# Optimization experiments

Measured on AMD Instinct MI355X. Metric: run time of the kernel, lower is better.

The kernel has to match this reference:

```python
import jax, jax.numpy as jnp
import numpy as np

EPS = 1e-07

def ternary_quantize(w, gamma=1.0):
    # gamma' = gamma / (mean|W| + eps)
    w_bar = jnp.mean(jnp.abs(w))
    gamma_prime = gamma / (w_bar + EPS)
    q = jnp.where(w > 0.5, 1.0, jnp.where(w < -0.5, -1.0, 0.0)).astype(w.dtype)
    # RoundClip(gamma' * q, -1, 1); jnp.round matches torch.round (half-to-even)
    return jnp.clip(jnp.round(gamma_prime * q), -1.0, 1.0)

def setup_inputs() -> dict:
    key = jax.random.key(0)
    kx, kw = jax.random.split(key)
    x = jax.random.normal(kx, (4, 2048, 4096), dtype=jnp.float32)
    weight = jax.random.normal(kw, (4096, 4096), dtype=jnp.float32)  # [out, in]
    return {"x": x, "weight": weight}

def reference(x, weight):
    wq = ternary_quantize(weight)
    # F.linear: x @ W^T
    return jnp.einsum('bsi,oi->bso', x, wq)
```

## Files before the change

### kernel.cpp

```cpp
#include <hip/hip_runtime.h>
#include <hip/hip_bf16.h>
#include <stdint.h>


typedef __bf16 bf16x8 __attribute__((ext_vector_type(8)));
typedef float  f32x4  __attribute__((ext_vector_type(4)));

#define EPS 1e-7f
#define NPART 4096

__device__ __forceinline__ void async_load16(const void* g, void* l) {
    __builtin_amdgcn_global_load_lds(
        (__attribute__((address_space(1))) void*)(const_cast<void*>(g)),
        (__attribute__((address_space(3))) void*)l,
        16, 0, 0);
}

__device__ __forceinline__ unsigned short f2bf_rne(float f) {
    unsigned u = __float_as_uint(f);
    unsigned r = (u + 0x7fffu + ((u >> 16) & 1u)) >> 16;
    return (unsigned short)r;
}

__device__ __forceinline__ float scale_from_partials(const float* __restrict__ partials,
                                                     float invCount) {
    const int lane = threadIdx.x & 63;
    const float4* p4 = (const float4*)partials;
    float s = 0.0f;
    #pragma unroll
    for (int j = 0; j < NPART / 4 / 64; ++j) {
        float4 v = p4[lane + 64 * j];
        s += v.x + v.y + v.z + v.w;
    }
    #pragma unroll
    for (int off = 32; off > 0; off >>= 1) s += __shfl_down(s, off, 64);
    s = __shfl(s, 0, 64);
    float mean = s * invCount;
    float gp = 1.0f / (mean + EPS);
    return fminf(fmaxf(rintf(gp), -1.0f), 1.0f);
}


__device__ __forceinline__ unsigned short tern_bf16(float w) {
    return (w > 0.5f) ? (unsigned short)0x3F80u
         : ((w < -0.5f) ? (unsigned short)0xBF80u : (unsigned short)0u);
}

__global__ __launch_bounds__(256) void quant_w_bf16(
    const float* __restrict__ in, ushort4* __restrict__ out,
    float* __restrict__ partials, int n4)
{
    int tid = blockIdx.x * blockDim.x + threadIdx.x;
    int stride = gridDim.x * blockDim.x;
    float s = 0.0f;
    for (int i = tid; i < n4; i += stride) {
        float4 v = ((const float4*)in)[i];
        s += fabsf(v.x) + fabsf(v.y) + fabsf(v.z) + fabsf(v.w);
        ushort4 r;
        r.x = tern_bf16(v.x); r.y = tern_bf16(v.y);
        r.z = tern_bf16(v.z); r.w = tern_bf16(v.w);
        out[i] = r;
    }
    #pragma unroll
    for (int off = 32; off > 0; off >>= 1) s += __shfl_down(s, off, 64);
    __shared__ float psum[4];
    int lane = threadIdx.x & 63, wid = threadIdx.x >> 6;
    if (lane == 0) psum[wid] = s;
    __syncthreads();
    if (threadIdx.x == 0)
        partials[blockIdx.x] = psum[0] + psum[1] + psum[2] + psum[3];
}


__global__ __launch_bounds__(256) void conv_x_bf16(
    const float* __restrict__ in, ushort4* __restrict__ out, int n4)
{
    int i = blockIdx.x * blockDim.x + threadIdx.x;
    if (i < n4) {
        float4 v = ((const float4*)in)[i];
        ushort4 r;
        r.x = f2bf_rne(v.x); r.y = f2bf_rne(v.y);
        r.z = f2bf_rne(v.z); r.w = f2bf_rne(v.w);
        out[i] = r;
    }
}


#define BM 128
#define BN 128
#define BK 64

__global__ __launch_bounds__(256) void gemm_bt(
    const __bf16* __restrict__ A,
    const __bf16* __restrict__ B,
    float* __restrict__ C,
    const float* __restrict__ partials,
    int N, int K, float invCount)
{
    __shared__ __bf16 As[BM * BK];
    __shared__ __bf16 Bs[BN * BK];

    const int t    = threadIdx.x;
    const int lane = t & 63;
    const int wid  = t >> 6;
    const int mBase = blockIdx.y * BM;
    const int nBase = blockIdx.x * BN;
    const int wm = (wid >> 1) * 64;
    const int wn = (wid & 1) * 64;
    const int lm = lane & 15;
    const int quad = lane >> 4;
    const int lm7 = lm & 7;

    f32x4 acc[4][4] = {};

    const __bf16* gA = A + (size_t)mBase * K;
    const __bf16* gB = B + (size_t)nBase * K;

    for (int k0 = 0; k0 < K; k0 += BK) {
        #pragma unroll
        for (int i = 0; i < 4; ++i) {
            int ch = i * 256 + t;
            int row = ch >> 3, sc = ch & 7;
            int cc = sc ^ (row & 7);
            async_load16(gA + (size_t)row * K + k0 + cc * 8, &As[ch * 8]);
        }
        #pragma unroll
        for (int i = 0; i < 4; ++i) {
            int ch = i * 256 + t;
            int row = ch >> 3, sc = ch & 7;
            int cc = sc ^ (row & 7);
            async_load16(gB + (size_t)row * K + k0 + cc * 8, &Bs[ch * 8]);
        }
        __syncthreads();

        #pragma unroll
        for (int ks = 0; ks < BK; ks += 32) {
            const int cc = (ks >> 3) + quad;
            const int swz = cc ^ lm7;
            bf16x8 af[4], bfr[4];
            #pragma unroll
            for (int mt = 0; mt < 4; ++mt)
                af[mt] = *(const bf16x8*)&As[((wm + mt * 16 + lm) * 8 + swz) * 8];
            #pragma unroll
            for (int nt = 0; nt < 4; ++nt)
                bfr[nt] = *(const bf16x8*)&Bs[((wn + nt * 16 + lm) * 8 + swz) * 8];
            #pragma unroll
            for (int mt = 0; mt < 4; ++mt)
                #pragma unroll
                for (int nt = 0; nt < 4; ++nt)
                    acc[mt][nt] = __builtin_amdgcn_mfma_f32_16x16x32_bf16(
                        af[mt], bfr[nt], acc[mt][nt], 0, 0, 0);
        }
        __syncthreads();
    }

    const float tscale = scale_from_partials(partials, invCount);

    #pragma unroll
    for (int mt = 0; mt < 4; ++mt) {
        #pragma unroll
        for (int nt = 0; nt < 4; ++nt) {
            #pragma unroll
            for (int r = 0; r < 4; ++r) {
                int row = mBase + wm + mt * 16 + quad * 4 + r;
                int col = nBase + wn + nt * 16 + lm;
                C[(size_t)row * N + col] = tscale * acc[mt][nt][r];
            }
        }
    }
}


__global__ void gemm_fallback(const float* __restrict__ x, const float* __restrict__ w,
                              float* __restrict__ out, const float* __restrict__ partials,
                              int N, int K, float invCount)
{
    __shared__ float xs[16][17];
    __shared__ float qs[16][17];
    int tx = threadIdx.x & 15;
    int ty = threadIdx.x >> 4;
    int row = blockIdx.y * 16 + ty;
    int col = blockIdx.x * 16 + tx;
    float acc = 0.0f;
    for (int k0 = 0; k0 < K; k0 += 16) {
        xs[ty][tx] = x[(size_t)row * K + k0 + tx];
        float wv = w[(size_t)(blockIdx.x * 16 + ty) * K + k0 + tx];
        qs[ty][tx] = (wv > 0.5f) ? 1.0f : ((wv < -0.5f) ? -1.0f : 0.0f);
        __syncthreads();
        #pragma unroll
        for (int j = 0; j < 16; ++j) acc += xs[ty][j] * qs[tx][j];
        __syncthreads();
    }
    float tscale = scale_from_partials(partials, invCount);
    out[(size_t)row * N + col] = tscale * acc;
}

__global__ __launch_bounds__(256) void absmean_only(
    const float* __restrict__ w, float* __restrict__ partials, int n4)
{
    int tid = blockIdx.x * blockDim.x + threadIdx.x;
    int stride = gridDim.x * blockDim.x;
    float s = 0.0f;
    for (int i = tid; i < n4; i += stride) {
        float4 v = ((const float4*)w)[i];
        s += fabsf(v.x) + fabsf(v.y) + fabsf(v.z) + fabsf(v.w);
    }
    #pragma unroll
    for (int off = 32; off > 0; off >>= 1) s += __shfl_down(s, off, 64);
    __shared__ float psum[4];
    int lane = threadIdx.x & 63, wid = threadIdx.x >> 6;
    if (lane == 0) psum[wid] = s;
    __syncthreads();
    if (threadIdx.x == 0)
        partials[blockIdx.x] = psum[0] + psum[1] + psum[2] + psum[3];
}


extern "C" void kernel_launch(void* const* d_in, const int* in_sizes, int n_in,
                              void* d_out, int out_size, void* d_ws, size_t ws_size,
                              hipStream_t stream) {
    const float* x = (const float*)d_in[0];
    const float* w = (const float*)d_in[1];
    float* out = (float*)d_out;

    const int K = 4096;
    const int M = in_sizes[0] / K;
    const int N = in_sizes[1] / K;
    const float invCount = 1.0f / (float)(in_sizes[1]);

    float* partials = (float*)d_ws;
    const size_t base = NPART * sizeof(float);
    const size_t need = base + (size_t)M * K * 2 + (size_t)N * K * 2;

    if (ws_size >= need) {
        __bf16* xb = (__bf16*)((char*)d_ws + base);
        __bf16* qb = (__bf16*)((char*)d_ws + base + (size_t)M * K * 2);

        int xn4 = (M * K) / 4;
        int wn4 = (N * K) / 4;
        quant_w_bf16<<<NPART, 256, 0, stream>>>(w, (ushort4*)qb, partials, wn4);
        conv_x_bf16<<<(xn4 + 255) / 256, 256, 0, stream>>>(x, (ushort4*)xb, xn4);

        dim3 grid(N / BN, M / BM);
        gemm_bt<<<grid, 256, 0, stream>>>(xb, qb, out, partials, N, K, invCount);
    } else {
        absmean_only<<<NPART, 256, 0, stream>>>(w, partials, in_sizes[1] / 4);
        dim3 grid(N / 16, M / 16);
        gemm_fallback<<<grid, 256, 0, stream>>>(x, w, out, partials, N, K, invCount);
    }
}
```

Before: 570.2 us.

## Use 32x32 MFMA, XCD-aware tile remap, and fuse prep kernels

The GEMM inner loop now uses the 32x32x16 bf16 MFMA with a 2x2 tile per wave instead of 4x4 16x16x32 tiles. This cuts LDS fragment loads per MFMA and raises work per instruction. Workgroups are remapped so that each XCD handles a contiguous band of N panels, which should improve L2 reuse of the weight tiles. The weight quantization and x conversion kernels are merged into one grid-stride prep kernel, saving a launch at the cost of a fixed grid size for the x conversion.

After: 667.1 us. 17.0% more time.

```diff
diff --git a/kernel.cpp b/kernel.cpp
--- a/kernel.cpp
+++ b/kernel.cpp
@@ -3,8 +3,8 @@
 #include <stdint.h>
 
 
-typedef __bf16 bf16x8 __attribute__((ext_vector_type(8)));
-typedef float  f32x4  __attribute__((ext_vector_type(4)));
+typedef __bf16 bf16x8  __attribute__((ext_vector_type(8)));
+typedef float  f32x16  __attribute__((ext_vector_type(16)));
 
 #define EPS 1e-7f
 #define NPART 4096
@@ -40,26 +40,34 @@
     return fminf(fmaxf(rintf(gp), -1.0f), 1.0f);
 }
 
-
 __device__ __forceinline__ unsigned short tern_bf16(float w) {
     return (w > 0.5f) ? (unsigned short)0x3F80u
          : ((w < -0.5f) ? (unsigned short)0xBF80u : (unsigned short)0u);
 }
 
-__global__ __launch_bounds__(256) void quant_w_bf16(
-    const float* __restrict__ in, ushort4* __restrict__ out,
-    float* __restrict__ partials, int n4)
+
+__global__ __launch_bounds__(256) void prep(
+    const float* __restrict__ x, const float* __restrict__ w,
+    ushort4* __restrict__ xb, ushort4* __restrict__ qb,
+    float* __restrict__ partials, int xn4, int wn4)
 {
     int tid = blockIdx.x * blockDim.x + threadIdx.x;
     int stride = gridDim.x * blockDim.x;
     float s = 0.0f;
-    for (int i = tid; i < n4; i += stride) {
-        float4 v = ((const float4*)in)[i];
+    for (int i = tid; i < wn4; i += stride) {
+        float4 v = ((const float4*)w)[i];
         s += fabsf(v.x) + fabsf(v.y) + fabsf(v.z) + fabsf(v.w);
         ushort4 r;
         r.x = tern_bf16(v.x); r.y = tern_bf16(v.y);
         r.z = tern_bf16(v.z); r.w = tern_bf16(v.w);
-        out[i] = r;
+        qb[i] = r;
+    }
+    for (int i = tid; i < xn4; i += stride) {
+        float4 v = ((const float4*)x)[i];
+        ushort4 r;
+        r.x = f2bf_rne(v.x); r.y = f2bf_rne(v.y);
+        r.z = f2bf_rne(v.z); r.w = f2bf_rne(v.w);
+        xb[i] = r;
     }
     #pragma unroll
     for (int off = 32; off > 0; off >>= 1) s += __shfl_down(s, off, 64);
@@ -72,20 +80,6 @@
 }
 
 
-__global__ __launch_bounds__(256) void conv_x_bf16(
-    const float* __restrict__ in, ushort4* __restrict__ out, int n4)
-{
-    int i = blockIdx.x * blockDim.x + threadIdx.x;
-    if (i < n4) {
-        float4 v = ((const float4*)in)[i];
-        ushort4 r;
-        r.x = f2bf_rne(v.x); r.y = f2bf_rne(v.y);
-        r.z = f2bf_rne(v.z); r.w = f2bf_rne(v.w);
-        out[i] = r;
-    }
-}
-
-
 #define BM 128
 #define BN 128
 #define BK 64
@@ -95,7 +89,7 @@
     const __bf16* __restrict__ B,
     float* __restrict__ C,
     const float* __restrict__ partials,
-    int N, int K, float invCount)
+    int N, int K, float invCount, int mPan, int nPan)
 {
     __shared__ __bf16 As[BM * BK];
     __shared__ __bf16 Bs[BN * BK];
@@ -103,15 +97,27 @@
     const int t    = threadIdx.x;
     const int lane = t & 63;
     const int wid  = t >> 6;
-    const int mBase = blockIdx.y * BM;
-    const int nBase = blockIdx.x * BN;
+
+    int gid = blockIdx.y * gridDim.x + blockIdx.x;
+    int mIdx, nIdx;
+    if ((nPan & 7) == 0 && ((mPan * nPan) & 7) == 0) {
+        int xcd = gid & 7;
+        int local = gid >> 3;
+        mIdx = local % mPan;
+        nIdx = xcd * (nPan >> 3) + (local / mPan);
+    } else {
+        nIdx = gid % nPan;
+        mIdx = gid / nPan;
+    }
+
+    const int mBase = mIdx * BM;
+    const int nBase = nIdx * BN;
     const int wm = (wid >> 1) * 64;
     const int wn = (wid & 1) * 64;
-    const int lm = lane & 15;
-    const int quad = lane >> 4;
-    const int lm7 = lm & 7;
-
-    f32x4 acc[4][4] = {};
+    const int l31   = lane & 31;
+    const int khalf = lane >> 5;
+
+    f32x16 acc[2][2] = {};
 
     const __bf16* gA = A + (size_t)mBase * K;
     const __bf16* gB = B + (size_t)nBase * K;
@@ -134,21 +140,24 @@
         __syncthreads();
 
         #pragma unroll
-        for (int ks = 0; ks < BK; ks += 32) {
-            const int cc = (ks >> 3) + quad;
-            const int swz = cc ^ lm7;
-            bf16x8 af[4], bfr[4];
-            #pragma unroll
-            for (int mt = 0; mt < 4; ++mt)
-                af[mt] = *(const bf16x8*)&As[((wm + mt * 16 + lm) * 8 + swz) * 8];
-            #pragma unroll
-            for (int nt = 0; nt < 4; ++nt)
-                bfr[nt] = *(const bf16x8*)&Bs[((wn + nt * 16 + lm) * 8 + swz) * 8];
-            #pragma unroll
-            for (int mt = 0; mt < 4; ++mt)
+        for (int ks = 0; ks < BK; ks += 16) {
+            const int cc = (ks >> 3) + khalf;
+            bf16x8 af[2], bfr[2];
+            #pragma unroll
+            for (int mt = 0; mt < 2; ++mt) {
+                int row = wm + mt * 32 + l31;
+                af[mt] = *(const bf16x8*)&As[(row * 8 + (cc ^ (row & 7))) * 8];
+            }
+            #pragma unroll
+            for (int nt = 0; nt < 2; ++nt) {
+                int row = wn + nt * 32 + l31;
+                bfr[nt] = *(const bf16x8*)&Bs[(row * 8 + (cc ^ (row & 7))) * 8];
+            }
+            #pragma unroll
+            for (int mt = 0; mt < 2; ++mt)
                 #pragma unroll
-                for (int nt = 0; nt < 4; ++nt)
-                    acc[mt][nt] = __builtin_amdgcn_mfma_f32_16x16x32_bf16(
+                for (int nt = 0; nt < 2; ++nt)
+                    acc[mt][nt] = __builtin_amdgcn_mfma_f32_32x32x16_bf16(
                         af[mt], bfr[nt], acc[mt][nt], 0, 0, 0);
         }
         __syncthreads();
@@ -157,13 +166,13 @@
     const float tscale = scale_from_partials(partials, invCount);
 
     #pragma unroll
-    for (int mt = 0; mt < 4; ++mt) {
-        #pragma unroll
-        for (int nt = 0; nt < 4; ++nt) {
-            #pragma unroll
-            for (int r = 0; r < 4; ++r) {
-                int row = mBase + wm + mt * 16 + quad * 4 + r;
-                int col = nBase + wn + nt * 16 + lm;
+    for (int mt = 0; mt < 2; ++mt) {
+        #pragma unroll
+        for (int nt = 0; nt < 2; ++nt) {
+            #pragma unroll
+            for (int r = 0; r < 16; ++r) {
+                int row = mBase + wm + mt * 32 + (r & 3) + 8 * (r >> 2) + 4 * khalf;
+                int col = nBase + wn + nt * 32 + l31;
                 C[(size_t)row * N + col] = tscale * acc[mt][nt][r];
             }
         }
@@ -238,11 +247,13 @@
 
         int xn4 = (M * K) / 4;
         int wn4 = (N * K) / 4;
-        quant_w_bf16<<<NPART, 256, 0, stream>>>(w, (ushort4*)qb, partials, wn4);
-        conv_x_bf16<<<(xn4 + 255) / 256, 256, 0, stream>>>(x, (ushort4*)xb, xn4);
-
-        dim3 grid(N / BN, M / BM);
-        gemm_bt<<<grid, 256, 0, stream>>>(xb, qb, out, partials, N, K, invCount);
+        prep<<<NPART, 256, 0, stream>>>(x, w, (ushort4*)xb, (ushort4*)qb,
+                                        partials, xn4, wn4);
+
+        int mPan = M / BM, nPan = N / BN;
+        dim3 grid(nPan, mPan);
+        gemm_bt<<<grid, 256, 0, stream>>>(xb, qb, out, partials, N, K, invCount,
+                                          mPan, nPan);
     } else {
         absmean_only<<<NPART, 256, 0, stream>>>(w, partials, in_sizes[1] / 4);
         dim3 grid(N / 16, M / 16);
```
